# Optimization experiments

Measured on AMD Instinct MI355X. Metric: run time of the kernel, lower is better.

The kernel has to match this reference:

```python
import jax, jax.numpy as jnp
import numpy as np

N_NODES = 100000
N_EDGES = 3200000
IN_DIM = 11
HID = 32


def setup_inputs() -> dict:
    key = jax.random.key(0)
    ks = jax.random.split(key, 12)
    inp = {
        "x": jax.random.normal(ks[0], (N_NODES, IN_DIM), dtype=jnp.float32),
        "edge_index": jax.random.randint(ks[1], (2, N_EDGES), 0, N_NODES, dtype=jnp.int32),
        "batch": jnp.zeros((N_NODES,), dtype=jnp.int32),
        # GCNConv layer 1 (11 -> 32)
        "W1": jax.random.normal(ks[2], (IN_DIM, HID), dtype=jnp.float32) / np.sqrt(IN_DIM),
        "b1": jnp.zeros((HID,), dtype=jnp.float32),
        # GCNConv layer 2 (32 -> 32)
        "W2": jax.random.normal(ks[3], (HID, HID), dtype=jnp.float32) / np.sqrt(HID),
        "b2": jnp.zeros((HID,), dtype=jnp.float32),
        # output MLP: 32 -> 16 -> 1
        "Wo1": jax.random.normal(ks[4], (HID, HID // 2), dtype=jnp.float32) / np.sqrt(HID),
        "bo1": jnp.zeros((HID // 2,), dtype=jnp.float32),
        "Wo2": jax.random.normal(ks[5], (HID // 2, 1), dtype=jnp.float32) / np.sqrt(HID // 2),
        "bo2": jnp.zeros((1,), dtype=jnp.float32),
    }
    return inp


def _gcn_norm(edge_index, n_nodes):
    # Add self-loops and compute symmetric normalization (PyG GCNConv default).
    loops = jnp.arange(n_nodes, dtype=edge_index.dtype)
    src = jnp.concatenate([edge_index[0], loops])
    dst = jnp.concatenate([edge_index[1], loops])
    ones = jnp.ones_like(dst, dtype=jnp.float32)
    deg = jax.ops.segment_sum(ones, dst, num_segments=n_nodes)  # degree of A+I on target side
    dinv = jax.lax.rsqrt(deg)  # deg >= 1 thanks to self-loops
    norm = dinv[src] * dinv[dst]  # [E+N]
    return src, dst, norm


def _gcn_conv(x, W, b, src, dst, norm, n_nodes):
    xw = x @ W                                   # transform first (small dim)
    msg = norm[:, None] * xw[src]                # gather + scale  [E+N, H]
    agg = jax.ops.segment_sum(msg, dst, num_segments=n_nodes)  # scatter-add
    return agg + b


def reference(x, edge_index, batch, W1, b1, W2, b2, Wo1, bo1, Wo2, bo2):
    n = x.shape[0]
    src, dst, norm = _gcn_norm(edge_index, n)
    h = jax.nn.relu(_gcn_conv(x, W1, b1, src, dst, norm, n))
    # F.dropout(training=self.training) is identity in eval mode
    h = jax.nn.relu(_gcn_conv(h, W2, b2, src, dst, norm, n))
    h = jax.nn.elu(h @ Wo1 + bo1)
    out = h @ Wo2 + bo2
    return out.squeeze(-1)  # [N]
```

## Files before the change

kernel.cpp:

```cpp
#include <hip/hip_runtime.h>
#include <hip/hip_fp16.h>
#include <math.h>

#define N_NODES 100000
#define N_EDGES 3200000
#define IN_DIM 11
#define HID 32
#define HID2 16
#define SCHUNK 100352
#define BINSHIFT 8
#define BINSZ 256
#define NB 391
#define CHUNK 6144
#define NCH 521
#define NCH1 522
#define FCAP 9216

__device__ __forceinline__ int wincl(int v) {
    int lane = threadIdx.x & 63;
#pragma unroll
    for (int d = 1; d < 64; d <<= 1) {
        int u = __shfl_up(v, d, 64);
        v += (lane >= d) ? u : 0;
    }
    return v;
}

__device__ __forceinline__ int blkexcl512(int v, int* wtot) {
    int t = threadIdx.x, lane = t & 63, w = t >> 6;
    int inc = wincl(v);
    if (lane == 63) wtot[w] = inc;
    __syncthreads();
    if (t < 8) {
        int x = wtot[t], ix = x;
#pragma unroll
        for (int d = 1; d < 8; d <<= 1) {
            int u = __shfl_up(ix, d, 64);
            ix += (lane >= d) ? u : 0;
        }
        wtot[t] = ix - x;
    }
    __syncthreads();
    return inc - v + wtot[w];
}

__global__ __launch_bounds__(256) void k_hist(const int* __restrict__ ei,
                                              int* __restrict__ cnthist) {
    __shared__ int h[NB];
    int t = threadIdx.x;
    for (int i = t; i < NB; i += 256) h[i] = 0;
    __syncthreads();
    int b0 = blockIdx.x * CHUNK;
    int n = N_EDGES - b0; if (n > CHUNK) n = CHUNK;
    for (int e = t * 4; e < n; e += 1024) {
        int4 d4 = *(const int4*)(ei + N_EDGES + b0 + e);
        atomicAdd(&h[d4.x >> BINSHIFT], 1);
        atomicAdd(&h[d4.y >> BINSHIFT], 1);
        atomicAdd(&h[d4.z >> BINSHIFT], 1);
        atomicAdd(&h[d4.w >> BINSHIFT], 1);
    }
    __syncthreads();
    for (int i = t; i < NB; i += 256)
        cnthist[i * NCH1 + blockIdx.x] = h[i];
}

__global__ __launch_bounds__(256) void k_colscan(int* __restrict__ cnthist,
                                                 int* __restrict__ colsum) {
    __shared__ int wtot[4];
    int i = blockIdx.x;
    int t = threadIdx.x;
    int lane = t & 63;
    int v[4];
    int s4 = 0;
#pragma unroll
    for (int u = 0; u < 4; ++u) {
        int idx = t * 4 + u;
        v[u] = (idx < NCH) ? cnthist[i * NCH1 + idx] : 0;
        s4 += v[u];
    }
    int inc = wincl(s4);
    if (lane == 63) wtot[t >> 6] = inc;
    __syncthreads();
    if (t < 4) {
        int x = wtot[t], ix = x;
#pragma unroll
        for (int d = 1; d < 4; d <<= 1) {
            int u2 = __shfl_up(ix, d, 64);
            ix += (lane >= d) ? u2 : 0;
        }
        wtot[t] = ix - x;
    }
    __syncthreads();
    int base = inc - s4 + wtot[t >> 6];
#pragma unroll
    for (int u = 0; u < 4; ++u) {
        int idx = t * 4 + u;
        if (idx < NCH) cnthist[i * NCH1 + idx] = base;
        base += v[u];
    }
    if (t == 255) {
        cnthist[i * NCH1 + NCH] = base;
        colsum[i] = base;
    }
}

__global__ __launch_bounds__(512) void k_scanbins(const int* __restrict__ colsum,
                                                  int* __restrict__ binbase) {
    __shared__ int wtot[8];
    int t = threadIdx.x;
    int v = (t < NB) ? colsum[t] : 0;
    int pre = blkexcl512(v, wtot);
    if (t < NB) binbase[t] = pre;
    if (t == 0) binbase[NB] = N_EDGES;
}

__global__ __launch_bounds__(512) void k_binscatter(const int* __restrict__ ei,
                                                    const int* __restrict__ binbase,
                                                    const int* __restrict__ cnthist,
                                                    unsigned* __restrict__ binbuf) {
    __shared__ unsigned       srecS[CHUNK];
    __shared__ unsigned short sbinS[CHUNK];
    __shared__ int h[NB], rl[NB], gb[NB];
    __shared__ int wtot[8];
    int t = threadIdx.x;
    int b0 = blockIdx.x * CHUNK;
    int n = N_EDGES - b0; if (n > CHUNK) n = CHUNK;
    int pre_b = 0, c = 0;
    if (t < NB) {
        pre_b = cnthist[t * NCH1 + blockIdx.x];
        c = cnthist[t * NCH1 + blockIdx.x + 1] - pre_b;
    }
    int rlv = blkexcl512(c, wtot);
    if (t < NB) {
        rl[t] = rlv;
        gb[t] = binbase[t] + pre_b;
        h[t] = 0;
    }
    __syncthreads();
    for (int e = t; e < n; e += 512) {
        int d = ei[N_EDGES + b0 + e];
        int s = ei[b0 + e];
        int b = d >> BINSHIFT;
        int p = rl[b] + atomicAdd(&h[b], 1);
        srecS[p] = (unsigned)s | ((unsigned)(d & (BINSZ - 1)) << 17);
        sbinS[p] = (unsigned short)b;
    }
    __syncthreads();
    for (int p = t; p < n; p += 512) {
        int b = sbinS[p];
        binbuf[gb[b] + (p - rl[b])] = srecS[p];
    }
}

__global__ __launch_bounds__(512) void k_binfill(const unsigned* __restrict__ binbuf,
                                                 const int* __restrict__ binbase,
                                                 int* __restrict__ rowstart,
                                                 float* __restrict__ dinv,
                                                 int* __restrict__ csr_src,
                                                 const float* __restrict__ x,
                                                 const float* __restrict__ W1,
                                                 __half* __restrict__ xwh1) {
    int bb = blockIdx.x;
    int b = bb >> 1;
    int half = bb & 1;
    int t = threadIdx.x;
    __shared__ unsigned srec[FCAP];
    __shared__ int cnt[BINSZ], rloc[BINSZ], cur[BINSZ], wtot[8];
    __shared__ float sW[IN_DIM * HID];
    __shared__ float sx[128 * IN_DIM];
    __shared__ float sdinv[128];
    int base_node = b * BINSZ + half * 128;
    for (int i = t; i < IN_DIM * HID; i += 512) sW[i] = W1[i];
    for (int i = t; i < 128 * IN_DIM; i += 512) {
        int gi = base_node * IN_DIM + i;
        if (gi < N_NODES * IN_DIM) sx[i] = x[gi];
    }
    int ebeg = binbase[b], eend = binbase[b + 1];
    int m = eend - ebeg;
    if (t < BINSZ) cnt[t] = 0;
    __syncthreads();
    for (int e = t; e < m; e += 512) {
        unsigned v = binbuf[ebeg + e];
        if (e < FCAP) srec[e] = v;
        atomicAdd(&cnt[v >> 17], 1);
    }
    __syncthreads();
    int c = (t < BINSZ) ? cnt[t] : 0;
    int pre = blkexcl512(c, wtot);
    if (t < BINSZ) {
        rloc[t] = pre;
        cur[t] = 0;
        int node = b * BINSZ + t;
        if ((t >> 7) == half && node < N_NODES) {
            rowstart[node] = ebeg + pre;
            float dd = rsqrtf((float)c + 1.0f);
            dinv[node] = dd;
            sdinv[t - half * 128] = dd;
        }
    }
    if (bb == 0 && t == 0) rowstart[N_NODES] = N_EDGES;
    __syncthreads();
    for (int e = t; e < m; e += 512) {
        unsigned vv = (e < FCAP) ? srec[e] : binbuf[ebeg + e];
        int dl = vv >> 17;
        if ((dl >> 7) == half) {
            int p = ebeg + rloc[dl] + atomicAdd(&cur[dl], 1);
            csr_src[p] = (int)(vv & 0x1FFFFu);
        }
    }
#pragma unroll
    for (int r = 0; r < 8; ++r) {
        int o = t + r * 512;
        int mm = o >> 5, j = o & 31;
        int node = base_node + mm;
        if (node < N_NODES) {
            float a = 0.0f;
#pragma unroll
            for (int k = 0; k < IN_DIM; ++k)
                a += sx[mm * IN_DIM + k] * sW[k * HID + j];
            xwh1[node * HID + j] = __float2half(sdinv[mm] * a);
        }
    }
}

__device__ __forceinline__ void accum8(float* __restrict__ acc, const uint4 v) {
    float2 f0 = __half22float2(*(const __half2*)&v.x);
    float2 f1 = __half22float2(*(const __half2*)&v.y);
    float2 f2 = __half22float2(*(const __half2*)&v.z);
    float2 f3 = __half22float2(*(const __half2*)&v.w);
    acc[0] += f0.x; acc[1] += f0.y;
    acc[2] += f1.x; acc[3] += f1.y;
    acc[4] += f2.x; acc[5] += f2.y;
    acc[6] += f3.x; acc[7] += f3.y;
}

__device__ __forceinline__ void edge_accum8(int beg, int end, int q, int oj,
                                            const int* __restrict__ csr_src,
                                            const __half* __restrict__ xwh,
                                            float* __restrict__ acc) {
#pragma unroll
    for (int k = 0; k < 8; ++k) acc[k] = 0.0f;
    int e = beg;
    for (; e + 32 <= end; e += 32) {
        int s0 = csr_src[e + q];
        int s1 = csr_src[e + 8 + q];
        int s2 = csr_src[e + 16 + q];
        int s3 = csr_src[e + 24 + q];
        uint4 v0 = *(const uint4*)(xwh + ((s0 << 5) | oj));
        uint4 v1 = *(const uint4*)(xwh + ((s1 << 5) | oj));
        uint4 v2 = *(const uint4*)(xwh + ((s2 << 5) | oj));
        uint4 v3 = *(const uint4*)(xwh + ((s3 << 5) | oj));
        accum8(acc, v0); accum8(acc, v1); accum8(acc, v2); accum8(acc, v3);
    }
    if (e + 16 <= end) {
        int s0 = csr_src[e + q];
        int s1 = csr_src[e + 8 + q];
        uint4 v0 = *(const uint4*)(xwh + ((s0 << 5) | oj));
        uint4 v1 = *(const uint4*)(xwh + ((s1 << 5) | oj));
        accum8(acc, v0); accum8(acc, v1);
        e += 16;
    }
    if (e + 8 <= end) {
        int s0 = csr_src[e + q];
        uint4 v0 = *(const uint4*)(xwh + ((s0 << 5) | oj));
        accum8(acc, v0);
        e += 8;
    }
    if (e + q < end) {
        int s0 = csr_src[e + q];
        uint4 v0 = *(const uint4*)(xwh + ((s0 << 5) | oj));
        accum8(acc, v0);
    }
#pragma unroll
    for (int m = 4; m <= 16; m <<= 1) {
#pragma unroll
        for (int k = 0; k < 8; ++k) acc[k] += __shfl_xor(acc[k], m);
    }
}

__global__ __launch_bounds__(256) void k_gather_xw2(const int* __restrict__ rowstart,
                                                    const float* __restrict__ dinv,
                                                    const int* __restrict__ csr_src,
                                                    const __half* __restrict__ xwh1,
                                                    const float* __restrict__ b1,
                                                    const float* __restrict__ W2,
                                                    __half* __restrict__ xwh2) {
    __shared__ float sW2[HID * HID];
    __shared__ float sA[8][33];
    __shared__ float sH[8][33];
    for (int i = threadIdx.x; i < HID * HID; i += 256) sW2[i] = W2[i];

    int ln = threadIdx.x >> 5;
    int node = blockIdx.x * 8 + ln;
    int l = threadIdx.x & 31;
    int q = l >> 2;
    int oj = (l & 3) << 3;

    float acc[8];
    edge_accum8(rowstart[node], rowstart[node + 1], q, oj, csr_src, xwh1, acc);
    if (q == 0) {
#pragma unroll
        for (int k = 0; k < 8; ++k) sA[ln][oj + k] = acc[k];
    }
    __syncthreads();

    int j = l;
    float dd = dinv[node];
    float hv = dd * (sA[ln][j] + __half2float(xwh1[node * HID + j])) + b1[j];
    sH[ln][j] = hv > 0.0f ? hv : 0.0f;
    __syncthreads();

    float a2 = 0.0f;
#pragma unroll
    for (int k = 0; k < HID; ++k) a2 += sH[ln][k] * sW2[k * HID + j];
    xwh2[node * HID + j] = __float2half(dd * a2);
}

__global__ __launch_bounds__(256) void k_gather_mlp(const int* __restrict__ rowstart,
                                                    const float* __restrict__ dinv,
                                                    const int* __restrict__ csr_src,
                                                    const __half* __restrict__ xwh,
                                                    const float* __restrict__ b2,
                                                    const float* __restrict__ Wo1,
                                                    const float* __restrict__ bo1,
                                                    const float* __restrict__ Wo2,
                                                    const float* __restrict__ bo2,
                                                    float* __restrict__ out) {
    __shared__ float sW1[HID * HID2];
    __shared__ float sb1[HID2];
    __shared__ float sW2v[HID2];
    __shared__ float sb2[HID];
    __shared__ float sA[8][33];
    __shared__ float sH[8][33];
    for (int i = threadIdx.x; i < HID * HID2; i += 256) sW1[i] = Wo1[i];
    if (threadIdx.x < HID2) {
        sb1[threadIdx.x] = bo1[threadIdx.x];
        sW2v[threadIdx.x] = Wo2[threadIdx.x];
    }
    if (threadIdx.x < HID) sb2[threadIdx.x] = b2[threadIdx.x];

    int ln = threadIdx.x >> 5;
    int node = blockIdx.x * 8 + ln;
    int l = threadIdx.x & 31;
    int q = l >> 2;
    int oj = (l & 3) << 3;

    float acc[8];
    edge_accum8(rowstart[node], rowstart[node + 1], q, oj, csr_src, xwh, acc);
    if (q == 0) {
#pragma unroll
        for (int k = 0; k < 8; ++k) sA[ln][oj + k] = acc[k];
    }
    __syncthreads();

    int j = l;
    float dd = dinv[node];
    float hv = dd * (sA[ln][j] + __half2float(xwh[node * HID + j])) + sb2[j];
    sH[ln][j] = hv > 0.0f ? hv : 0.0f;
    __syncthreads();

    float val = 0.0f;
    if (j < HID2) {
        float a = sb1[j];
#pragma unroll
        for (int k = 0; k < HID; ++k) a += sH[ln][k] * sW1[k * HID2 + j];
        a = a > 0.0f ? a : (expf(a) - 1.0f);
        val = a * sW2v[j];
    }
#pragma unroll
    for (int d = 16; d >= 1; d >>= 1) val += __shfl_down(val, d, 32);
    if (j == 0) out[node] = val + bo2[0];
}

extern "C" void kernel_launch(void* const* d_in, const int* in_sizes, int n_in,
                              void* d_out, int out_size, void* d_ws, size_t ws_size,
                              hipStream_t stream) {
    const float* x   = (const float*)d_in[0];
    const int*   ei  = (const int*)d_in[1];
    const float* W1  = (const float*)d_in[3];
    const float* b1  = (const float*)d_in[4];
    const float* W2  = (const float*)d_in[5];
    const float* b2  = (const float*)d_in[6];
    const float* Wo1 = (const float*)d_in[7];
    const float* bo1 = (const float*)d_in[8];
    const float* Wo2 = (const float*)d_in[9];
    const float* bo2 = (const float*)d_in[10];
    float* out = (float*)d_out;

    int*      colsum   = (int*)d_ws;
    int*      binbase  = colsum + 512;
    int*      rowstart = binbase + 512;
    float*    dinv     = (float*)(rowstart + SCHUNK);
    int*      csr_src  = (int*)(dinv + SCHUNK);
    unsigned* binbuf   = (unsigned*)(csr_src + N_EDGES);
    __half*   XWH1     = (__half*)(binbuf + N_EDGES);
    __half*   XWH2     = XWH1 + (size_t)N_NODES * HID;
    int*      cnthist  = csr_src;

    const int BT = 256;
    int gG = N_NODES / 8;

    k_hist      <<<NCH, BT, 0, stream>>>(ei, cnthist);
    k_colscan   <<<NB, BT, 0, stream>>>(cnthist, colsum);
    k_scanbins  <<<1, 512, 0, stream>>>(colsum, binbase);
    k_binscatter<<<NCH, 512, 0, stream>>>(ei, binbase, cnthist, binbuf);
    k_binfill   <<<2 * NB, 512, 0, stream>>>(binbuf, binbase, rowstart, dinv,
                                             csr_src, x, W1, XWH1);

    k_gather_xw2<<<gG, BT, 0, stream>>>(rowstart, dinv, csr_src, XWH1, b1, W2, XWH2);

    k_gather_mlp<<<gG, BT, 0, stream>>>(rowstart, dinv, csr_src, XWH2,
                                        b2, Wo1, bo1, Wo2, bo2, out);
}
```

Baseline: 238.9 us.

## Split feature tables into half planes and stage edge indices in LDS per block

Node features are stored as two 16-wide fp16 planes instead of one 32-wide row, and each gather block handles 50 nodes. The block first loads its contiguous CSR index range into shared memory, then gathers the low plane for all its nodes and then the high plane. The aim is to shrink the random-access working set per pass so it stays cache resident, and to replace repeated global index loads with LDS reads. The cost is two passes over the edges, more shared memory per block, and an occupancy hint of 8 blocks per CU.

```diff
diff --git a/kernel.cpp b/kernel.cpp
--- a/kernel.cpp
+++ b/kernel.cpp
@@ -15,6 +15,9 @@
 #define NCH 521
 #define NCH1 522
 #define FCAP 9216
+#define GBLK 2000
+#define GNODES 50
+#define SIDXCAP 2176
 
 __device__ __forceinline__ int wincl(int v) {
     int lane = threadIdx.x & 63;
@@ -208,6 +211,8 @@
             csr_src[p] = (int)(vv & 0x1FFFFu);
         }
     }
+    __half* xl = xwh1;
+    __half* xh = xwh1 + (size_t)N_NODES * 16;
 #pragma unroll
     for (int r = 0; r < 8; ++r) {
         int o = t + r * 512;
@@ -218,7 +223,9 @@
 #pragma unroll
             for (int k = 0; k < IN_DIM; ++k)
                 a += sx[mm * IN_DIM + k] * sW[k * HID + j];
-            xwh1[node * HID + j] = __float2half(sdinv[mm] * a);
+            __half hv = __float2half(sdinv[mm] * a);
+            if (j < 16) xl[node * 16 + j] = hv;
+            else        xh[node * 16 + (j - 16)] = hv;
         }
     }
 }
@@ -234,142 +241,234 @@
     acc[6] += f3.x; acc[7] += f3.y;
 }
 
-__device__ __forceinline__ void edge_accum8(int beg, int end, int q, int oj,
-                                            const int* __restrict__ csr_src,
-                                            const __half* __restrict__ xwh,
-                                            float* __restrict__ acc) {
-#pragma unroll
-    for (int k = 0; k < 8; ++k) acc[k] = 0.0f;
+__device__ __forceinline__ void edge_range16(int beg, int end, int q, int oj,
+                                             const int* __restrict__ sidx,
+                                             const __half* __restrict__ plane,
+                                             float* __restrict__ acc) {
     int e = beg;
     for (; e + 32 <= end; e += 32) {
-        int s0 = csr_src[e + q];
-        int s1 = csr_src[e + 8 + q];
-        int s2 = csr_src[e + 16 + q];
-        int s3 = csr_src[e + 24 + q];
-        uint4 v0 = *(const uint4*)(xwh + ((s0 << 5) | oj));
-        uint4 v1 = *(const uint4*)(xwh + ((s1 << 5) | oj));
-        uint4 v2 = *(const uint4*)(xwh + ((s2 << 5) | oj));
-        uint4 v3 = *(const uint4*)(xwh + ((s3 << 5) | oj));
-        accum8(acc, v0); accum8(acc, v1); accum8(acc, v2); accum8(acc, v3);
+        int s0 = sidx[e + q];
+        int s1 = sidx[e + 16 + q];
+        uint4 v0 = *(const uint4*)(plane + ((s0 << 4) | oj));
+        uint4 v1 = *(const uint4*)(plane + ((s1 << 4) | oj));
+        accum8(acc, v0); accum8(acc, v1);
     }
     if (e + 16 <= end) {
-        int s0 = csr_src[e + q];
-        int s1 = csr_src[e + 8 + q];
-        uint4 v0 = *(const uint4*)(xwh + ((s0 << 5) | oj));
-        uint4 v1 = *(const uint4*)(xwh + ((s1 << 5) | oj));
-        accum8(acc, v0); accum8(acc, v1);
+        int s0 = sidx[e + q];
+        uint4 v0 = *(const uint4*)(plane + ((s0 << 4) | oj));
+        accum8(acc, v0);
         e += 16;
     }
-    if (e + 8 <= end) {
-        int s0 = csr_src[e + q];
-        uint4 v0 = *(const uint4*)(xwh + ((s0 << 5) | oj));
+    if (e + q < end) {
+        int s0 = sidx[e + q];
+        uint4 v0 = *(const uint4*)(plane + ((s0 << 4) | oj));
         accum8(acc, v0);
-        e += 8;
+    }
+}
+
+__device__ __forceinline__ void edge_range16g(int beg, int end, int q, int oj,
+                                              const int* __restrict__ csr,
+                                              const __half* __restrict__ plane,
+                                              float* __restrict__ acc) {
+    int e = beg;
+    for (; e + 16 <= end; e += 16) {
+        int s0 = csr[e + q];
+        uint4 v0 = *(const uint4*)(plane + ((s0 << 4) | oj));
+        accum8(acc, v0);
     }
     if (e + q < end) {
-        int s0 = csr_src[e + q];
-        uint4 v0 = *(const uint4*)(xwh + ((s0 << 5) | oj));
+        int s0 = csr[e + q];
+        uint4 v0 = *(const uint4*)(plane + ((s0 << 4) | oj));
         accum8(acc, v0);
     }
-#pragma unroll
-    for (int m = 4; m <= 16; m <<= 1) {
-#pragma unroll
-        for (int k = 0; k < 8; ++k) acc[k] += __shfl_xor(acc[k], m);
-    }
-}
-
-__global__ __launch_bounds__(256) void k_gather_xw2(const int* __restrict__ rowstart,
-                                                    const float* __restrict__ dinv,
-                                                    const int* __restrict__ csr_src,
-                                                    const __half* __restrict__ xwh1,
-                                                    const float* __restrict__ b1,
-                                                    const float* __restrict__ W2,
-                                                    __half* __restrict__ xwh2) {
+}
+
+__device__ __forceinline__ void octet_reduce16(float* __restrict__ acc) {
+#pragma unroll
+    for (int m2 = 2; m2 <= 16; m2 <<= 1) {
+#pragma unroll
+        for (int k = 0; k < 8; ++k) acc[k] += __shfl_xor(acc[k], m2);
+    }
+}
+
+#define GROUNDS ((GNODES + 7) / 8)
+
+__device__ __forceinline__ void phase_gather(const __half* __restrict__ plane,
+                                             const int* __restrict__ srow,
+                                             const int* __restrict__ sidx,
+                                             const int* __restrict__ csr_src,
+                                             int ebase, int g, int q, int oj, int l,
+                                             float (*sA)[16]) {
+#pragma unroll 1
+    for (int r = 0; r < GROUNDS; ++r) {
+        int idx = r * 8 + g;
+        if (idx < GNODES) {
+            int rel0 = srow[idx], rel1 = srow[idx + 1];
+            float acc[8];
+#pragma unroll
+            for (int k = 0; k < 8; ++k) acc[k] = 0.0f;
+            if (rel1 <= SIDXCAP)
+                edge_range16(rel0, rel1, q, oj, sidx, plane, acc);
+            else
+                edge_range16g(ebase + rel0, ebase + rel1, q, oj, csr_src, plane, acc);
+            octet_reduce16(acc);
+            if (l < 2) {
+#pragma unroll
+                for (int k = 0; k < 8; ++k) sA[idx][l * 8 + k] = acc[k];
+            }
+        }
+    }
+}
+
+__global__ __launch_bounds__(256, 8) void k_gather_xw2(const int* __restrict__ rowstart,
+                                                       const float* __restrict__ dinv,
+                                                       const int* __restrict__ csr_src,
+                                                       const __half* __restrict__ xwh1,
+                                                       const float* __restrict__ b1,
+                                                       const float* __restrict__ W2,
+                                                       __half* __restrict__ xwh2) {
+    __shared__ int   sidx[SIDXCAP];
+    __shared__ int   srow[GNODES + 1];
+    __shared__ float sAlo[GNODES][16];
+    __shared__ float sAhi[GNODES][16];
     __shared__ float sW2[HID * HID];
-    __shared__ float sA[8][33];
-    __shared__ float sH[8][33];
-    for (int i = threadIdx.x; i < HID * HID; i += 256) sW2[i] = W2[i];
-
-    int ln = threadIdx.x >> 5;
-    int node = blockIdx.x * 8 + ln;
-    int l = threadIdx.x & 31;
-    int q = l >> 2;
-    int oj = (l & 3) << 3;
-
-    float acc[8];
-    edge_accum8(rowstart[node], rowstart[node + 1], q, oj, csr_src, xwh1, acc);
-    if (q == 0) {
-#pragma unroll
-        for (int k = 0; k < 8; ++k) sA[ln][oj + k] = acc[k];
-    }
-    __syncthreads();
-
-    int j = l;
-    float dd = dinv[node];
-    float hv = dd * (sA[ln][j] + __half2float(xwh1[node * HID + j])) + b1[j];
-    sH[ln][j] = hv > 0.0f ? hv : 0.0f;
-    __syncthreads();
-
-    float a2 = 0.0f;
-#pragma unroll
-    for (int k = 0; k < HID; ++k) a2 += sH[ln][k] * sW2[k * HID + j];
-    xwh2[node * HID + j] = __float2half(dd * a2);
-}
-
-__global__ __launch_bounds__(256) void k_gather_mlp(const int* __restrict__ rowstart,
-                                                    const float* __restrict__ dinv,
-                                                    const int* __restrict__ csr_src,
-                                                    const __half* __restrict__ xwh,
-                                                    const float* __restrict__ b2,
-                                                    const float* __restrict__ Wo1,
-                                                    const float* __restrict__ bo1,
-                                                    const float* __restrict__ Wo2,
-                                                    const float* __restrict__ bo2,
-                                                    float* __restrict__ out) {
+    __shared__ float sb1[HID];
+    int t = threadIdx.x;
+    int nb0 = blockIdx.x * GNODES;
+    const __half* p1lo = xwh1;
+    const __half* p1hi = xwh1 + (size_t)N_NODES * 16;
+    __half* p2lo = xwh2;
+    __half* p2hi = xwh2 + (size_t)N_NODES * 16;
+
+    for (int i = t; i < HID * HID; i += 256) sW2[i] = W2[i];
+    if (t < HID) sb1[t] = b1[t];
+    int ebase = rowstart[nb0];
+    for (int i = t; i <= GNODES; i += 256) srow[i] = rowstart[nb0 + i] - ebase;
+    __syncthreads();
+    int nblk = srow[GNODES]; if (nblk > SIDXCAP) nblk = SIDXCAP;
+    for (int i = t; i < nblk; i += 256)
+        sidx[i] = __builtin_nontemporal_load(csr_src + ebase + i);
+    __syncthreads();
+
+    int g = t >> 5;
+    int l = t & 31;
+    int q = l >> 1;
+    int oj = (l & 1) << 3;
+
+    phase_gather(p1lo, srow, sidx, csr_src, ebase, g, q, oj, l, sAlo);
+    __syncthreads();
+#pragma unroll 1
+    for (int r = 0; r < GROUNDS; ++r) {
+        int idx = r * 8 + g;
+        if (idx < GNODES) {
+            int rel0 = srow[idx], rel1 = srow[idx + 1];
+            float acc[8];
+#pragma unroll
+            for (int k = 0; k < 8; ++k) acc[k] = 0.0f;
+            if (rel1 <= SIDXCAP)
+                edge_range16(rel0, rel1, q, oj, sidx, p1hi, acc);
+            else
+                edge_range16g(ebase + rel0, ebase + rel1, q, oj, csr_src, p1hi, acc);
+            octet_reduce16(acc);
+            if (l < 2) {
+#pragma unroll
+                for (int k = 0; k < 8; ++k) sAhi[idx][l * 8 + k] = acc[k];
+            }
+            int node = nb0 + idx;
+            float aj = (l < 16) ? sAlo[idx][l] : sAhi[idx][l - 16];
+            float selfv = __half2float((l < 16) ? p1lo[node * 16 + l]
+                                                : p1hi[node * 16 + (l - 16)]);
+            float dd = dinv[node];
+            float hv = dd * (aj + selfv) + sb1[l];
+            hv = hv > 0.0f ? hv : 0.0f;
+            float a2 = 0.0f;
+#pragma unroll
+            for (int k = 0; k < HID; ++k)
+                a2 += __shfl(hv, k, 32) * sW2[k * HID + l];
+            __half o = __float2half(dd * a2);
+            if (l < 16) p2lo[node * 16 + l] = o;
+            else        p2hi[node * 16 + (l - 16)] = o;
+        }
+    }
+}
+
+__global__ __launch_bounds__(256, 8) void k_gather_mlp(const int* __restrict__ rowstart,
+                                                       const float* __restrict__ dinv,
+                                                       const int* __restrict__ csr_src,
+                                                       const __half* __restrict__ xwh,
+                                                       const float* __restrict__ b2,
+                                                       const float* __restrict__ Wo1,
+                                                       const float* __restrict__ bo1,
+                                                       const float* __restrict__ Wo2,
+                                                       const float* __restrict__ bo2,
+                                                       float* __restrict__ out) {
+    __shared__ int   sidx[SIDXCAP];
+    __shared__ int   srow[GNODES + 1];
+    __shared__ float sAlo[GNODES][16];
+    __shared__ float sAhi[GNODES][16];
     __shared__ float sW1[HID * HID2];
     __shared__ float sb1[HID2];
     __shared__ float sW2v[HID2];
     __shared__ float sb2[HID];
-    __shared__ float sA[8][33];
-    __shared__ float sH[8][33];
-    for (int i = threadIdx.x; i < HID * HID2; i += 256) sW1[i] = Wo1[i];
-    if (threadIdx.x < HID2) {
-        sb1[threadIdx.x] = bo1[threadIdx.x];
-        sW2v[threadIdx.x] = Wo2[threadIdx.x];
-    }
-    if (threadIdx.x < HID) sb2[threadIdx.x] = b2[threadIdx.x];
-
-    int ln = threadIdx.x >> 5;
-    int node = blockIdx.x * 8 + ln;
-    int l = threadIdx.x & 31;
-    int q = l >> 2;
-    int oj = (l & 3) << 3;
-
-    float acc[8];
-    edge_accum8(rowstart[node], rowstart[node + 1], q, oj, csr_src, xwh, acc);
-    if (q == 0) {
-#pragma unroll
-        for (int k = 0; k < 8; ++k) sA[ln][oj + k] = acc[k];
-    }
-    __syncthreads();
-
-    int j = l;
-    float dd = dinv[node];
-    float hv = dd * (sA[ln][j] + __half2float(xwh[node * HID + j])) + sb2[j];
-    sH[ln][j] = hv > 0.0f ? hv : 0.0f;
-    __syncthreads();
-
-    float val = 0.0f;
-    if (j < HID2) {
-        float a = sb1[j];
-#pragma unroll
-        for (int k = 0; k < HID; ++k) a += sH[ln][k] * sW1[k * HID2 + j];
-        a = a > 0.0f ? a : (expf(a) - 1.0f);
-        val = a * sW2v[j];
-    }
-#pragma unroll
-    for (int d = 16; d >= 1; d >>= 1) val += __shfl_down(val, d, 32);
-    if (j == 0) out[node] = val + bo2[0];
+    int t = threadIdx.x;
+    int nb0 = blockIdx.x * GNODES;
+    const __half* plo = xwh;
+    const __half* phi = xwh + (size_t)N_NODES * 16;
+
+    for (int i = t; i < HID * HID2; i += 256) sW1[i] = Wo1[i];
+    if (t < HID2) { sb1[t] = bo1[t]; sW2v[t] = Wo2[t]; }
+    if (t < HID) sb2[t] = b2[t];
+    int ebase = rowstart[nb0];
+    for (int i = t; i <= GNODES; i += 256) srow[i] = rowstart[nb0 + i] - ebase;
+    __syncthreads();
+    int nblk = srow[GNODES]; if (nblk > SIDXCAP) nblk = SIDXCAP;
+    for (int i = t; i < nblk; i += 256)
+        sidx[i] = __builtin_nontemporal_load(csr_src + ebase + i);
+    __syncthreads();
+
+    int g = t >> 5;
+    int l = t & 31;
+    int q = l >> 1;
+    int oj = (l & 1) << 3;
+
+    phase_gather(plo, srow, sidx, csr_src, ebase, g, q, oj, l, sAlo);
+    __syncthreads();
+#pragma unroll 1
+    for (int r = 0; r < GROUNDS; ++r) {
+        int idx = r * 8 + g;
+        if (idx < GNODES) {
+            int rel0 = srow[idx], rel1 = srow[idx + 1];
+            float acc[8];
+#pragma unroll
+            for (int k = 0; k < 8; ++k) acc[k] = 0.0f;
+            if (rel1 <= SIDXCAP)
+                edge_range16(rel0, rel1, q, oj, sidx, phi, acc);
+            else
+                edge_range16g(ebase + rel0, ebase + rel1, q, oj, csr_src, phi, acc);
+            octet_reduce16(acc);
+            if (l < 2) {
+#pragma unroll
+                for (int k = 0; k < 8; ++k) sAhi[idx][l * 8 + k] = acc[k];
+            }
+            int node = nb0 + idx;
+            float aj = (l < 16) ? sAlo[idx][l] : sAhi[idx][l - 16];
+            float selfv = __half2float((l < 16) ? plo[node * 16 + l]
+                                                : phi[node * 16 + (l - 16)]);
+            float dd = dinv[node];
+            float hv = dd * (aj + selfv) + sb2[l];
+            hv = hv > 0.0f ? hv : 0.0f;
+            int j = l & 15;
+            float a = sb1[j];
+#pragma unroll
+            for (int k = 0; k < HID; ++k)
+                a += __shfl(hv, k, 32) * sW1[k * HID2 + j];
+            a = a > 0.0f ? a : (expf(a) - 1.0f);
+            float val = (l < HID2) ? a * sW2v[j] : 0.0f;
+#pragma unroll
+            for (int d = 16; d >= 1; d >>= 1) val += __shfl_down(val, d, 32);
+            if (l == 0) out[node] = val + bo2[0];
+        }
+    }
 }
 
 extern "C" void kernel_launch(void* const* d_in, const int* in_sizes, int n_in,
@@ -398,7 +497,6 @@
     int*      cnthist  = csr_src;
 
     const int BT = 256;
-    int gG = N_NODES / 8;
 
     k_hist      <<<NCH, BT, 0, stream>>>(ei, cnthist);
     k_colscan   <<<NB, BT, 0, stream>>>(cnthist, colsum);
@@ -407,8 +505,8 @@
     k_binfill   <<<2 * NB, 512, 0, stream>>>(binbuf, binbase, rowstart, dinv,
                                              csr_src, x, W1, XWH1);
 
-    k_gather_xw2<<<gG, BT, 0, stream>>>(rowstart, dinv, csr_src, XWH1, b1, W2, XWH2);
-
-    k_gather_mlp<<<gG, BT, 0, stream>>>(rowstart, dinv, csr_src, XWH2,
-                                        b2, Wo1, bo1, Wo2, bo2, out);
-}
+    k_gather_xw2<<<GBLK, BT, 0, stream>>>(rowstart, dinv, csr_src, XWH1, b1, W2, XWH2);
+
+    k_gather_mlp<<<GBLK, BT, 0, stream>>>(rowstart, dinv, csr_src, XWH2,
+                                          b2, Wo1, bo1, Wo2, bo2, out);
+}
```

Result: slower. 297.3 us (+24.4%).
